# Performance work log

Measured on AMD Instinct MI355X. Metric: run time of the kernel, lower is better.

Reference implementation:

```python
import jax, jax.numpy as jnp
import numpy as np

B, T, N_EMBD, HEAD = 8, 2048, 1024, 64

def setup_inputs() -> dict:
    key = jax.random.key(0)
    kx, kk, kq, kv = jax.random.split(key, 4)
    x = jax.random.normal(kx, (B, T, N_EMBD), dtype=jnp.float32)
    Wk = jax.random.normal(kk, (HEAD, N_EMBD), dtype=jnp.float32) * 0.02
    Wq = jax.random.normal(kq, (HEAD, N_EMBD), dtype=jnp.float32) * 0.02
    Wv = jax.random.normal(kv, (HEAD, N_EMBD), dtype=jnp.float32) * 0.02
    return {"x": x, "Wk": Wk, "Wq": Wq, "Wv": Wv}

def reference(x, Wk, Wq, Wv):
    # x: [B, T, C]; Linear(n_embd, head_size, bias=False) => x @ W.T
    Bq, Tq, C = x.shape
    q = jnp.einsum('btc,hc->bth', x, Wq)  # [B, T, H]
    k = jnp.einsum('btc,hc->bth', x, Wk)
    v = jnp.einsum('btc,hc->bth', x, Wv)
    # NOTE: source scales by C**0.5 with C = n_embd (not head_size); preserved.
    scale = 1.0 / jnp.sqrt(jnp.float32(C))
    wei = jnp.einsum('bth,bsh->bts', q, k) * scale  # [B, T, T]
    # causal mask: allow key position s <= query position t
    causal = jnp.tril(jnp.ones((Tq, Tq), dtype=bool))
    wei = jnp.where(causal[None, :, :], wei, -jnp.inf)
    wei = jax.nn.softmax(wei, axis=-1)
    # dropout is identity at inference
    out = jnp.einsum('bts,bsh->bth', wei, v)  # [B, T, H]
    return out
```

## Files before the change

### kernel.cpp

```cpp
#include <hip/hip_runtime.h>

#define TB 2048
#define NB 8
#define CEMB 1024
#define HD 64
#define BT (NB*TB)
#define QSCALE 0.04508422f

typedef __attribute__((ext_vector_type(8))) short bf16x8;
typedef __attribute__((ext_vector_type(4))) short bf16x4;
typedef __attribute__((ext_vector_type(4))) float f32x4;

#define MFMA32(a, b, c) __builtin_amdgcn_mfma_f32_16x16x32_bf16(a, b, c, 0, 0, 0)
#define MFMA16(a, b, c) __builtin_amdgcn_mfma_f32_16x16x16bf16_1k(a, b, c, 0, 0, 0)

__device__ inline short f2bf(float f) {
    union { float f; unsigned u; } v; v.f = f;
    unsigned r = v.u + 0x7fffu + ((v.u >> 16) & 1u);
    return (short)(r >> 16);
}
__device__ inline float bf2f(short s) {
    union { unsigned u; float f; } v; v.u = ((unsigned)(unsigned short)s) << 16;
    return v.f;
}
__device__ inline unsigned cvt_pk_bf16(float a, float b) {
    unsigned r;
    asm("v_cvt_pk_bf16_f32 %0, %1, %2" : "=v"(r) : "v"(a), "v"(b));
    return r;
}
__device__ inline bf16x4 pack2(unsigned w0, unsigned w1) {
    union { unsigned u[2]; bf16x4 v; } c; c.u[0] = w0; c.u[1] = w1; return c.v;
}
__device__ inline bf16x8 pack4(unsigned w0, unsigned w1, unsigned w2, unsigned w3) {
    union { unsigned u[4]; bf16x8 v; } c;
    c.u[0] = w0; c.u[1] = w1; c.u[2] = w2; c.u[3] = w3; return c.v;
}
__device__ inline void gload_lds16(const void* g, void* l) {
    __builtin_amdgcn_global_load_lds((const __attribute__((address_space(1))) void*)g,
                                     (__attribute__((address_space(3))) void*)l, 16, 0, 0);
}

__global__ __launch_bounds__(256) void wpack(const float* __restrict__ Wk,
                                             const float* __restrict__ Wq,
                                             const float* __restrict__ Wv,
                                             short* __restrict__ W2) {
    int c = blockIdx.x * 256 + threadIdx.x;
    int lane = c & 63, ntk = c >> 6;
    int nt = ntk % 12, kc = ntk / 12;
    int n = nt * 16 + (lane & 15);
    int col = kc * 32 + (lane >> 4) * 8;
    const float* src = (n < 64) ? Wk + n * 1024
                     : (n < 128) ? Wq + (n - 64) * 1024
                                 : Wv + (n - 128) * 1024;
    float4 a = *(const float4*)(src + col);
    float4 b = *(const float4*)(src + col + 4);
    bf16x8 o;
    o[0] = f2bf(a.x); o[1] = f2bf(a.y); o[2] = f2bf(a.z); o[3] = f2bf(a.w);
    o[4] = f2bf(b.x); o[5] = f2bf(b.y); o[6] = f2bf(b.z); o[7] = f2bf(b.w);
    *(bf16x8*)(W2 + (size_t)c * 8) = o;
}

__global__ __launch_bounds__(512) void qkv_proj(const float* __restrict__ x,
                                                const short* __restrict__ W2,
                                                short* __restrict__ Qb,
                                                short* __restrict__ Kb,
                                                short* __restrict__ Vt) {
    __shared__ __align__(16) char xbuf[2][16384];
    int tid = threadIdx.x, wid = tid >> 6, lane = tid & 63;
    int l15 = lane & 15, quad = lane >> 4;
    int mgrp = wid >> 2;
    int ngrp = wid & 3;
    int m0 = blockIdx.x * 64;

    f32x4 acc[2][3];
#pragma unroll
    for (int i = 0; i < 2; ++i)
#pragma unroll
        for (int j = 0; j < 3; ++j) acc[i][j] = f32x4{0.f, 0.f, 0.f, 0.f};

    int ld4 = lane >> 4;
    const char* gs0; const char* gs1;
    {
        int r0 = (wid * 2) * 4 + ld4;
        int r1 = (wid * 2 + 1) * 4 + ld4;
        int sz0 = ((r0 & 3) << 5) | ((r0 & 4) << 2);
        int sz1 = ((r1 & 3) << 5) | ((r1 & 4) << 2);
        gs0 = (const char*)x + ((size_t)(m0 + r0) << 12) + ((l15 * 16) ^ sz0);
        gs1 = (const char*)x + ((size_t)(m0 + r1) << 12) + ((l15 * 16) ^ sz1);
    }
#define STAGE(bsel, t) do { \
        gload_lds16(gs0 + (t) * 256, &xbuf[bsel][(wid * 2) * 1024]);     \
        gload_lds16(gs1 + (t) * 256, &xbuf[bsel][(wid * 2 + 1) * 1024]); } while (0)

    int lrowA = mgrp * 32 + l15;
    int szr = ((lrowA & 3) << 5) | ((lrowA & 4) << 2);
    int baseA = lrowA * 256;
    int baseB = baseA + 4096;

    const short* wnt = W2 + (size_t)(ngrp * 3) * 512 + (size_t)lane * 8;

    STAGE(0, 0);
    for (int t = 0; t < 16; ++t) {
        bf16x8 wfj[3][2];
        {
            const short* ws = wnt + (size_t)(2 * t) * 6144;
#pragma unroll
            for (int j = 0; j < 3; ++j) {
                wfj[j][0] = *(const bf16x8*)(ws + j * 512);
                wfj[j][1] = *(const bf16x8*)(ws + j * 512 + 6144);
            }
        }
        if (t < 15) {
            STAGE((t + 1) & 1, t + 1);
            asm volatile("s_waitcnt vmcnt(8)" ::: "memory");
        } else {
            asm volatile("s_waitcnt vmcnt(6)" ::: "memory");
        }
        __builtin_amdgcn_s_barrier();

        const char* bp = &xbuf[t & 1][0];
        bf16x8 af[2][2];
#pragma unroll
        for (int kh = 0; kh < 2; ++kh) {
            int b0 = kh * 128 + quad * 32;
            float4 a0 = *(const float4*)(bp + baseA + ((b0) ^ szr));
            float4 a1 = *(const float4*)(bp + baseA + ((b0 + 16) ^ szr));
            float4 c0 = *(const float4*)(bp + baseB + ((b0) ^ szr));
            float4 c1 = *(const float4*)(bp + baseB + ((b0 + 16) ^ szr));
            af[0][kh] = pack4(cvt_pk_bf16(a0.x, a0.y), cvt_pk_bf16(a0.z, a0.w),
                              cvt_pk_bf16(a1.x, a1.y), cvt_pk_bf16(a1.z, a1.w));
            af[1][kh] = pack4(cvt_pk_bf16(c0.x, c0.y), cvt_pk_bf16(c0.z, c0.w),
                              cvt_pk_bf16(c1.x, c1.y), cvt_pk_bf16(c1.z, c1.w));
        }
#pragma unroll
        for (int kh = 0; kh < 2; ++kh)
#pragma unroll
            for (int j = 0; j < 3; ++j) {
                acc[0][j] = MFMA32(af[0][kh], wfj[j][kh], acc[0][j]);
                acc[1][j] = MFMA32(af[1][kh], wfj[j][kh], acc[1][j]);
            }
        __builtin_amdgcn_s_barrier();
    }
#undef STAGE

    int blk = blockIdx.x;
    int bb = blk >> 5;
    int inb = blk & 31;
#pragma unroll
    for (int j = 0; j < 3; ++j) {
        int gnt = ngrp * 3 + j;
#pragma unroll
        for (int mt = 0; mt < 2; ++mt) {
            int gmt = mgrp * 2 + mt;
            f32x4 s0 = acc[mt][j];
            int row0 = m0 + gmt * 16 + quad * 4;
            if (gnt < 4) {
                int h = gnt * 16 + l15;
#pragma unroll
                for (int r = 0; r < 4; ++r)
                    Kb[(size_t)(row0 + r) * HD + h] = f2bf(s0[r]);
            } else if (gnt < 8) {
                int h = (gnt - 4) * 16 + l15;
#pragma unroll
                for (int r = 0; r < 4; ++r)
                    Qb[(size_t)(row0 + r) * HD + h] = f2bf(s0[r] * QSCALE);
            } else {
                int h = (gnt - 8) * 16 + l15;
                int sblk32 = inb * 2 + (gmt >> 1);
                int half = gmt & 1;
                uint2 v2;
                v2.x = cvt_pk_bf16(s0[0], s0[1]);
                v2.y = cvt_pk_bf16(s0[2], s0[3]);
                *(uint2*)(Vt + ((size_t)((bb * 64 + sblk32) * 64 + h)) * 32
                             + quad * 8 + half * 4) = v2;
            }
        }
    }
}

__global__ __launch_bounds__(256) void flash(const short* __restrict__ Qb,
                                             const short* __restrict__ Kb,
                                             const short* __restrict__ Vt,
                                             float* __restrict__ out) {
    __shared__ float Of[4][2][16][68];
    __shared__ float Ml[4][2][16];
    int tid = threadIdx.x, wave = tid >> 6, lane = tid & 63;
    int l15 = lane & 15, quad = lane >> 4;
    int i = blockIdx.x;
    int round = i >> 8, s = i & 255;
    int b = s & 7;
    int g32 = s >> 3;
    int q32 = round ? 63 - g32 : g32;
    int tq0 = q32 * 32;
    size_t bT = (size_t)b * TB;

    const short* qr0 = Qb + (bT + tq0 + l15) * HD;
    const short* qr1 = Qb + (bT + tq0 + 16 + l15) * HD;
    bf16x8 qf00 = *(const bf16x8*)(qr0 + quad * 8);
    bf16x8 qf01 = *(const bf16x8*)(qr0 + 32 + quad * 8);
    bf16x8 qf10 = *(const bf16x8*)(qr1 + quad * 8);
    bf16x8 qf11 = *(const bf16x8*)(qr1 + 32 + quad * 8);

    bf16x4 ones4;
#pragma unroll
    for (int j = 0; j < 4; ++j) ones4[j] = (short)0x3F80;

    f32x4 accO0[4], accO1[4];
#pragma unroll
    for (int k = 0; k < 4; ++k) { accO0[k] = f32x4{0.f,0.f,0.f,0.f}; accO1[k] = f32x4{0.f,0.f,0.f,0.f}; }
    f32x4 accL0 = f32x4{0.f,0.f,0.f,0.f}, accL1 = f32x4{0.f,0.f,0.f,0.f};

    int ntiles = (tq0 + 95) >> 6;
    const short* kbase = Kb + bT * HD;
    const short* vtb = Vt + (size_t)b * 131072;

    int myt = wave;
    if (myt < ntiles) {
        bf16x8 kf[8];
        {
            const short* kr = kbase + (size_t)(myt * 64 + l15) * HD + quad * 8;
#pragma unroll
            for (int st = 0; st < 4; ++st) {
                kf[st * 2]     = *(const bf16x8*)(kr + (size_t)st * 16 * HD);
                kf[st * 2 + 1] = *(const bf16x8*)(kr + (size_t)st * 16 * HD + 32);
            }
        }
        for (; myt < ntiles; myt += 4) {
            int s0 = myt * 64;
            bf16x8 vf8[8];
#pragma unroll
            for (int sb2 = 0; sb2 < 2; ++sb2)
#pragma unroll
                for (int ht = 0; ht < 4; ++ht)
                    vf8[sb2 * 4 + ht] = *(const bf16x8*)(
                        vtb + ((size_t)(((s0 >> 5) + sb2) * 64 + ht * 16 + l15)) * 32 + quad * 8);
            f32x4 sv0[4], sv1[4];
            __builtin_amdgcn_s_setprio(1);
#pragma unroll
            for (int st = 0; st < 4; ++st) {
                f32x4 t0 = f32x4{0.f,0.f,0.f,0.f}, t1 = f32x4{0.f,0.f,0.f,0.f};
                t0 = MFMA32(kf[st * 2], qf00, t0);
                t0 = MFMA32(kf[st * 2 + 1], qf01, t0);
                t1 = MFMA32(kf[st * 2], qf10, t1);
                t1 = MFMA32(kf[st * 2 + 1], qf11, t1);
                sv0[st] = t0; sv1[st] = t1;
            }
            __builtin_amdgcn_s_setprio(0);
            if (myt + 4 < ntiles) {
                const short* kr = kbase + (size_t)(s0 + 256 + l15) * HD + quad * 8;
#pragma unroll
                for (int st = 0; st < 4; ++st) {
                    kf[st * 2]     = *(const bf16x8*)(kr + (size_t)st * 16 * HD);
                    kf[st * 2 + 1] = *(const bf16x8*)(kr + (size_t)st * 16 * HD + 32);
                }
            }
            bf16x4 pk0[4], pk1[4];
            if (s0 + 63 <= tq0) {
#pragma unroll
                for (int st = 0; st < 4; ++st) {
                    unsigned w00 = cvt_pk_bf16(__builtin_amdgcn_exp2f(sv0[st][0]),
                                               __builtin_amdgcn_exp2f(sv0[st][1]));
                    unsigned w01 = cvt_pk_bf16(__builtin_amdgcn_exp2f(sv0[st][2]),
                                               __builtin_amdgcn_exp2f(sv0[st][3]));
                    unsigned w10 = cvt_pk_bf16(__builtin_amdgcn_exp2f(sv1[st][0]),
                                               __builtin_amdgcn_exp2f(sv1[st][1]));
                    unsigned w11 = cvt_pk_bf16(__builtin_amdgcn_exp2f(sv1[st][2]),
                                               __builtin_amdgcn_exp2f(sv1[st][3]));
                    pk0[st] = pack2(w00, w01);
                    pk1[st] = pack2(w10, w11);
                }
            } else {
                int t0g = tq0 + l15, t1g = tq0 + 16 + l15;
#pragma unroll
                for (int st = 0; st < 4; ++st) {
                    bool full0 = (s0 + st * 16 + 15 <= tq0);
                    bool full1 = (s0 + st * 16 + 15 <= tq0 + 16);
                    int sb = s0 + st * 16 + quad * 4;
                    float a0 = (full0 || sb + 0 <= t0g) ? __builtin_amdgcn_exp2f(sv0[st][0]) : 0.f;
                    float a1 = (full0 || sb + 1 <= t0g) ? __builtin_amdgcn_exp2f(sv0[st][1]) : 0.f;
                    float a2 = (full0 || sb + 2 <= t0g) ? __builtin_amdgcn_exp2f(sv0[st][2]) : 0.f;
                    float a3 = (full0 || sb + 3 <= t0g) ? __builtin_amdgcn_exp2f(sv0[st][3]) : 0.f;
                    float c0 = (full1 || sb + 0 <= t1g) ? __builtin_amdgcn_exp2f(sv1[st][0]) : 0.f;
                    float c1 = (full1 || sb + 1 <= t1g) ? __builtin_amdgcn_exp2f(sv1[st][1]) : 0.f;
                    float c2 = (full1 || sb + 2 <= t1g) ? __builtin_amdgcn_exp2f(sv1[st][2]) : 0.f;
                    float c3 = (full1 || sb + 3 <= t1g) ? __builtin_amdgcn_exp2f(sv1[st][3]) : 0.f;
                    pk0[st] = pack2(cvt_pk_bf16(a0, a1), cvt_pk_bf16(a2, a3));
                    pk1[st] = pack2(cvt_pk_bf16(c0, c1), cvt_pk_bf16(c2, c3));
                }
            }
            __builtin_amdgcn_s_setprio(1);
#pragma unroll
            for (int g = 0; g < 4; ++g) {
                accL0 = MFMA16(ones4, pk0[g], accL0);
                accL1 = MFMA16(ones4, pk1[g], accL1);
#pragma unroll
                for (int ht = 0; ht < 4; ++ht) {
                    bf16x8 v = vf8[(g >> 1) * 4 + ht];
                    bf16x4 va;
                    if (g & 1) { va[0] = v[4]; va[1] = v[5]; va[2] = v[6]; va[3] = v[7]; }
                    else       { va[0] = v[0]; va[1] = v[1]; va[2] = v[2]; va[3] = v[3]; }
                    accO0[ht] = MFMA16(va, pk0[g], accO0[ht]);
                    accO1[ht] = MFMA16(va, pk1[g], accO1[ht]);
                }
            }
            __builtin_amdgcn_s_setprio(0);
        }
    }

#pragma unroll
    for (int ht = 0; ht < 4; ++ht) {
        float4 o0, o1;
        o0.x = accO0[ht][0]; o0.y = accO0[ht][1]; o0.z = accO0[ht][2]; o0.w = accO0[ht][3];
        o1.x = accO1[ht][0]; o1.y = accO1[ht][1]; o1.z = accO1[ht][2]; o1.w = accO1[ht][3];
        *(float4*)&Of[wave][0][l15][ht * 16 + quad * 4] = o0;
        *(float4*)&Of[wave][1][l15][ht * 16 + quad * 4] = o1;
    }
    if (quad == 0) { Ml[wave][0][l15] = accL0[0]; Ml[wave][1][l15] = accL1[0]; }
    __syncthreads();

    int row = tid >> 4, c4 = (tid & 15) * 4;
#pragma unroll
    for (int qt = 0; qt < 2; ++qt) {
        float L = Ml[0][qt][row] + Ml[1][qt][row] + Ml[2][qt][row] + Ml[3][qt][row];
        float inv = 1.0f / L;
        float4 p0 = *(const float4*)&Of[0][qt][row][c4];
        float4 p1 = *(const float4*)&Of[1][qt][row][c4];
        float4 p2 = *(const float4*)&Of[2][qt][row][c4];
        float4 p3 = *(const float4*)&Of[3][qt][row][c4];
        float4 o;
        o.x = (p0.x + p1.x + p2.x + p3.x) * inv;
        o.y = (p0.y + p1.y + p2.y + p3.y) * inv;
        o.z = (p0.z + p1.z + p2.z + p3.z) * inv;
        o.w = (p0.w + p1.w + p2.w + p3.w) * inv;
        *(float4*)(out + (bT + tq0 + qt * 16 + row) * HD + c4) = o;
    }
}

extern "C" void kernel_launch(void* const* d_in, const int* in_sizes, int n_in,
                              void* d_out, int out_size, void* d_ws, size_t ws_size,
                              hipStream_t stream) {
    const float* x  = (const float*)d_in[0];
    const float* Wk = (const float*)d_in[1];
    const float* Wq = (const float*)d_in[2];
    const float* Wv = (const float*)d_in[3];
    float* out = (float*)d_out;

    short* W2 = (short*)d_ws;
    short* Qb = W2 + 192 * 1024;
    short* Kb = Qb + (size_t)BT * HD;
    short* Vt = Kb + (size_t)BT * HD;

    wpack<<<96, 256, 0, stream>>>(Wk, Wq, Wv, W2);
    qkv_proj<<<256, 512, 0, stream>>>(x, W2, Qb, Kb, Vt);
    flash<<<512, 256, 0, stream>>>(Qb, Kb, Vt, out);
}
```

Baseline: 136.4 us.

## Stage weights through LDS with triple-buffered async loads in QKV projection

The QKV projection kernel now stages the bf16 weight tiles into shared memory through direct global-to-LDS loads, alongside the x tiles. Previously each wave loaded them from global memory into registers. The buffering goes from double to triple, with two stages prefetched ahead, and the LDS swizzle for x is simplified. The aim is to hide global load latency and cut redundant weight traffic across waves. In exchange, LDS use grows from 32KB to about 120KB per block, which may limit occupancy.

```diff
diff --git a/kernel.cpp b/kernel.cpp
--- a/kernel.cpp
+++ b/kernel.cpp
@@ -65,7 +65,8 @@
                                                 short* __restrict__ Qb,
                                                 short* __restrict__ Kb,
                                                 short* __restrict__ Vt) {
-    __shared__ __align__(16) char xbuf[2][16384];
+    __shared__ __align__(16) char xbuf[3][16384];
+    __shared__ __align__(16) char wbuf[3][24576];
     int tid = threadIdx.x, wid = tid >> 6, lane = tid & 63;
     int l15 = lane & 15, quad = lane >> 4;
     int mgrp = wid >> 2;
@@ -78,66 +79,65 @@
 #pragma unroll
         for (int j = 0; j < 3; ++j) acc[i][j] = f32x4{0.f, 0.f, 0.f, 0.f};
 
-    int ld4 = lane >> 4;
-    const char* gs0; const char* gs1;
-    {
-        int r0 = (wid * 2) * 4 + ld4;
-        int r1 = (wid * 2 + 1) * 4 + ld4;
-        int sz0 = ((r0 & 3) << 5) | ((r0 & 4) << 2);
-        int sz1 = ((r1 & 3) << 5) | ((r1 & 4) << 2);
-        gs0 = (const char*)x + ((size_t)(m0 + r0) << 12) + ((l15 * 16) ^ sz0);
-        gs1 = (const char*)x + ((size_t)(m0 + r1) << 12) + ((l15 * 16) ^ sz1);
-    }
+    int xr0 = wid * 8 + quad;
+    int xr1 = wid * 8 + 4 + quad;
+    const char* xs0 = (const char*)x + ((size_t)(m0 + xr0) << 12)
+                    + ((l15 * 16) ^ ((xr0 & 7) << 4));
+    const char* xs1 = (const char*)x + ((size_t)(m0 + xr1) << 12)
+                    + ((l15 * 16) ^ ((xr1 & 7) << 4));
+    const char* wsrc = (const char*)W2 + (size_t)(wid * 3) * 1024 + lane * 16;
+
 #define STAGE(bsel, t) do { \
-        gload_lds16(gs0 + (t) * 256, &xbuf[bsel][(wid * 2) * 1024]);     \
-        gload_lds16(gs1 + (t) * 256, &xbuf[bsel][(wid * 2 + 1) * 1024]); } while (0)
-
-    int lrowA = mgrp * 32 + l15;
-    int szr = ((lrowA & 3) << 5) | ((lrowA & 4) << 2);
-    int baseA = lrowA * 256;
-    int baseB = baseA + 4096;
-
-    const short* wnt = W2 + (size_t)(ngrp * 3) * 512 + (size_t)lane * 8;
+        gload_lds16(xs0 + (t) * 256, &xbuf[bsel][wid * 2048]);                      \
+        gload_lds16(xs1 + (t) * 256, &xbuf[bsel][wid * 2048 + 1024]);               \
+        gload_lds16(wsrc + (size_t)(t) * 24576,        &wbuf[bsel][wid * 3072]);        \
+        gload_lds16(wsrc + (size_t)(t) * 24576 + 1024, &wbuf[bsel][wid * 3072 + 1024]); \
+        gload_lds16(wsrc + (size_t)(t) * 24576 + 2048, &wbuf[bsel][wid * 3072 + 2048]); } while (0)
 
     STAGE(0, 0);
+    STAGE(1, 1);
+    int sw = (l15 & 7) << 4;
+#pragma unroll
     for (int t = 0; t < 16; ++t) {
-        bf16x8 wfj[3][2];
+        if (t < 14) {
+            STAGE((t + 2) % 3, t + 2);
+            asm volatile("s_waitcnt vmcnt(10)" ::: "memory");
+        } else if (t == 14) {
+            asm volatile("s_waitcnt vmcnt(5)" ::: "memory");
+        } else {
+            asm volatile("s_waitcnt vmcnt(0)" ::: "memory");
+        }
+        __builtin_amdgcn_s_barrier();
+        __builtin_amdgcn_sched_barrier(0);
+
+        const char* xb = xbuf[t % 3];
+        const char* wb = wbuf[t % 3];
+        bf16x8 wf[2][3];
         {
-            const short* ws = wnt + (size_t)(2 * t) * 6144;
+            const char* wbn = wb + (size_t)(ngrp * 3) * 1024 + lane * 16;
 #pragma unroll
             for (int j = 0; j < 3; ++j) {
-                wfj[j][0] = *(const bf16x8*)(ws + j * 512);
-                wfj[j][1] = *(const bf16x8*)(ws + j * 512 + 6144);
-            }
-        }
-        if (t < 15) {
-            STAGE((t + 1) & 1, t + 1);
-            asm volatile("s_waitcnt vmcnt(8)" ::: "memory");
-        } else {
-            asm volatile("s_waitcnt vmcnt(6)" ::: "memory");
-        }
-        __builtin_amdgcn_s_barrier();
-
-        const char* bp = &xbuf[t & 1][0];
+                wf[0][j] = *(const bf16x8*)(wbn + j * 1024);
+                wf[1][j] = *(const bf16x8*)(wbn + j * 1024 + 12288);
+            }
+        }
         bf16x8 af[2][2];
 #pragma unroll
-        for (int kh = 0; kh < 2; ++kh) {
-            int b0 = kh * 128 + quad * 32;
-            float4 a0 = *(const float4*)(bp + baseA + ((b0) ^ szr));
-            float4 a1 = *(const float4*)(bp + baseA + ((b0 + 16) ^ szr));
-            float4 c0 = *(const float4*)(bp + baseB + ((b0) ^ szr));
-            float4 c1 = *(const float4*)(bp + baseB + ((b0 + 16) ^ szr));
-            af[0][kh] = pack4(cvt_pk_bf16(a0.x, a0.y), cvt_pk_bf16(a0.z, a0.w),
-                              cvt_pk_bf16(a1.x, a1.y), cvt_pk_bf16(a1.z, a1.w));
-            af[1][kh] = pack4(cvt_pk_bf16(c0.x, c0.y), cvt_pk_bf16(c0.z, c0.w),
-                              cvt_pk_bf16(c1.x, c1.y), cvt_pk_bf16(c1.z, c1.w));
-        }
-#pragma unroll
-        for (int kh = 0; kh < 2; ++kh)
+        for (int mt = 0; mt < 2; ++mt)
+#pragma unroll
+            for (int kk = 0; kk < 2; ++kk) {
+                const char* xr = xb + (mgrp * 32 + mt * 16 + l15) * 256 + kk * 128;
+                float4 a0 = *(const float4*)(xr + ((quad * 32) ^ sw));
+                float4 a1 = *(const float4*)(xr + ((quad * 32 + 16) ^ sw));
+                af[mt][kk] = pack4(cvt_pk_bf16(a0.x, a0.y), cvt_pk_bf16(a0.z, a0.w),
+                                   cvt_pk_bf16(a1.x, a1.y), cvt_pk_bf16(a1.z, a1.w));
+            }
+#pragma unroll
+        for (int kk = 0; kk < 2; ++kk)
 #pragma unroll
             for (int j = 0; j < 3; ++j) {
-                acc[0][j] = MFMA32(af[0][kh], wfj[j][kh], acc[0][j]);
-                acc[1][j] = MFMA32(af[1][kh], wfj[j][kh], acc[1][j]);
+                acc[0][j] = MFMA32(af[0][kk], wf[kk][j], acc[0][j]);
+                acc[1][j] = MFMA32(af[1][kk], wf[kk][j], acc[1][j]);
             }
         __builtin_amdgcn_s_barrier();
     }
```

After: 131.5 us, median of 3. 3.6% less time.
